# Kernel tuning notes

Measured on AMD Instinct MI355X. Metric: run time of the kernel, lower is better.

Reference implementation:

```python
import jax, jax.numpy as jnp
import numpy as np

N_NODES = 50000
N_EDGES = 600000
D = 128
DROP_P = 0.5


def setup_inputs() -> dict:
    key = jax.random.key(0)
    k1, k2, k3, k4, k5, k6 = jax.random.split(key, 6)
    x = jax.random.normal(k1, (N_NODES, D), dtype=jnp.float32)
    W = jax.random.normal(k2, (D, D), dtype=jnp.float32) * (1.0 / np.sqrt(D))
    b = jax.random.normal(k3, (D,), dtype=jnp.float32) * 0.01
    mask_u = jax.random.uniform(k4, (N_NODES, D), dtype=jnp.float32)
    src = jax.random.randint(k5, (N_EDGES,), 0, N_NODES, dtype=jnp.int64)
    dst = jax.random.randint(k6, (N_EDGES,), 0, N_NODES, dtype=jnp.int64)
    return {"x": x, "W": W, "b": b, "mask_u": mask_u, "src": src, "dst": dst}


def reference(x, W, b, mask_u, src, dst):
    n_nodes = x.shape[0]
    # linear + relu (nn.Linear stores weight as [out, in]; here W is [out, in])
    h = jax.nn.relu(jnp.einsum('nd,od->no', x, W) + b)
    # inverted dropout with precomputed uniform noise (train mode, p=0.5)
    keep = (mask_u >= DROP_P).astype(h.dtype)
    h = h * keep * (1.0 / (1.0 - DROP_P))
    # message passing: msg = h[src], reduce = sum over incoming edges per dst
    msgs = jnp.take(h, src, axis=0)            # [E, D] gather
    out = jax.ops.segment_sum(msgs, dst, num_segments=n_nodes)  # [N, D]
    return out
```

## Files before the change

### kernel.cpp

```cpp
#include <hip/hip_runtime.h>

#define D 128
#define TILE_N 16
#define HPITCH 132
#define CAP 32
#define SPILL_MAX 8192

typedef __attribute__((ext_vector_type(8))) short  short8;
typedef __attribute__((ext_vector_type(4))) float  f32x4;

__device__ inline unsigned short f32_to_bf16(float f) {
    unsigned int u = __float_as_uint(f);
    unsigned int r = (u + 0x7FFFu + ((u >> 16) & 1u)) >> 16;
    return (unsigned short)r;
}
__device__ inline float bf16_to_f32(unsigned short s) {
    return __uint_as_float(((unsigned int)s) << 16);
}
__device__ inline short8 pack_bf16x8(float4 a, float4 b) {
    short8 u;
    u[0] = (short)f32_to_bf16(a.x); u[1] = (short)f32_to_bf16(a.y);
    u[2] = (short)f32_to_bf16(a.z); u[3] = (short)f32_to_bf16(a.w);
    u[4] = (short)f32_to_bf16(b.x); u[5] = (short)f32_to_bf16(b.y);
    u[6] = (short)f32_to_bf16(b.z); u[7] = (short)f32_to_bf16(b.w);
    return u;
}

__global__ __launch_bounds__(256) void prep_kernel(
    const float* __restrict__ W, unsigned short* __restrict__ Wb,
    const float* __restrict__ x, unsigned short* __restrict__ xb,
    const float* __restrict__ mask_u, unsigned char* __restrict__ mbits,
    int* __restrict__ cnt, int n_nodes, int* __restrict__ spill_cnt)
{
    const int tid = blockIdx.x * 256 + threadIdx.x;
    const int nth = gridDim.x * 256;

    for (int i = tid; i < (D * D) / 8; i += nth) {
        float4 v0 = *(const float4*)&W[i * 8];
        float4 v1 = *(const float4*)&W[i * 8 + 4];
        *(short8*)&Wb[i * 8] = pack_bf16x8(v0, v1);
    }
    const int nx8 = n_nodes * (D / 8);
    for (int i = tid; i < nx8; i += nth) {
        float4 v0 = *(const float4*)&x[(size_t)i * 8];
        float4 v1 = *(const float4*)&x[(size_t)i * 8 + 4];
        *(short8*)&xb[(size_t)i * 8] = pack_bf16x8(v0, v1);
    }
    for (int i = tid; i < nx8; i += nth) {
        float4 m0 = *(const float4*)&mask_u[(size_t)i * 8];
        float4 m1 = *(const float4*)&mask_u[(size_t)i * 8 + 4];
        unsigned b = 0;
        b |= (m0.x >= 0.5f) ? 1u : 0u;   b |= (m0.y >= 0.5f) ? 2u : 0u;
        b |= (m0.z >= 0.5f) ? 4u : 0u;   b |= (m0.w >= 0.5f) ? 8u : 0u;
        b |= (m1.x >= 0.5f) ? 16u : 0u;  b |= (m1.y >= 0.5f) ? 32u : 0u;
        b |= (m1.z >= 0.5f) ? 64u : 0u;  b |= (m1.w >= 0.5f) ? 128u : 0u;
        mbits[i] = (unsigned char)b;
    }
    for (int i = tid; i < n_nodes; i += nth) cnt[i] = 0;
    if (tid == 0 && spill_cnt) *spill_cnt = 0;
}

__global__ __launch_bounds__(256, 8) void gemm_mfma_kernel(
    const unsigned short* __restrict__ xb, const unsigned short* __restrict__ Wb,
    const float* __restrict__ bias, const unsigned char* __restrict__ mbits,
    unsigned short* __restrict__ h, int n_nodes,
    const int* __restrict__ src, const int* __restrict__ dst, int n_edges,
    int* __restrict__ cnt, unsigned short* __restrict__ bucket,
    int* __restrict__ spill_cnt, int* __restrict__ spill)
{
    __shared__ unsigned short ht[TILE_N * HPITCH];
    const int t    = threadIdx.x;
    const int lane = t & 63;
    const int w    = t >> 6;
    const int fr   = lane & 15;
    const int fg   = lane >> 4;
    const int n0 = blockIdx.x * TILE_N;

    const int e0 = blockIdx.x * 256 + t;
    int e_dst = 0, e_src = 0;
    const bool has_e0 = (e0 < n_edges);
    if (has_e0) { e_dst = dst[e0]; e_src = src[e0]; }

    const int prow = t >> 4;
    const int pcg  = t & 15;
    const int pnode = n0 + prow;
    const bool pvalid = (pnode < n_nodes);
    unsigned mbyte = 0;
    if (pvalid) mbyte = mbits[pnode * 16 + pcg];

    int arow = n0 + fr;
    if (arow >= n_nodes) arow = n_nodes - 1;
    const unsigned short* xr = xb + (size_t)arow * D;
    short8 a0 = *(const short8*)&xr[ 0 + fg * 8];
    short8 a1 = *(const short8*)&xr[32 + fg * 8];
    short8 a2 = *(const short8*)&xr[64 + fg * 8];
    short8 a3 = *(const short8*)&xr[96 + fg * 8];

    const float bs0 = bias[32 * w + fr];
    const float bs1 = bias[32 * w + 16 + fr];

    const unsigned short* wb0 = Wb + (size_t)(32 * w + fr) * D;
    const unsigned short* wb1 = Wb + (size_t)(32 * w + 16 + fr) * D;

    f32x4 acc0 = (f32x4){0.f, 0.f, 0.f, 0.f};
    f32x4 acc1 = (f32x4){0.f, 0.f, 0.f, 0.f};
    #pragma unroll
    for (int s = 0; s < 4; ++s) {
        short8 a = (s == 0) ? a0 : (s == 1) ? a1 : (s == 2) ? a2 : a3;
        short8 b0 = *(const short8*)&wb0[s * 32 + fg * 8];
        short8 b1 = *(const short8*)&wb1[s * 32 + fg * 8];
        acc0 = __builtin_amdgcn_mfma_f32_16x16x32_bf16(a, b0, acc0, 0, 0, 0);
        acc1 = __builtin_amdgcn_mfma_f32_16x16x32_bf16(a, b1, acc1, 0, 0, 0);
    }

    #pragma unroll
    for (int r = 0; r < 4; ++r) {
        const int rl = fg * 4 + r;
        float v0 = fmaxf(acc0[r] + bs0, 0.f);
        float v1 = fmaxf(acc1[r] + bs1, 0.f);
        ht[rl * HPITCH + 32 * w + fr]      = f32_to_bf16(v0);
        ht[rl * HPITCH + 32 * w + 16 + fr] = f32_to_bf16(v1);
    }
    __syncthreads();

    if (has_e0) {
        int pos = atomicAdd(&cnt[e_dst], 1);
        if (pos < CAP) {
            bucket[(size_t)e_dst * CAP + pos] = (unsigned short)e_src;
        } else {
            int k = atomicAdd(spill_cnt, 1);
            if (k < SPILL_MAX) { spill[2 * k] = e_dst; spill[2 * k + 1] = e_src; }
        }
    }
    const int stride = gridDim.x * 256;
    for (int i = e0 + stride; i < n_edges; i += stride) {
        int dd  = dst[i];
        int ss  = src[i];
        int pos = atomicAdd(&cnt[dd], 1);
        if (pos < CAP) {
            bucket[(size_t)dd * CAP + pos] = (unsigned short)ss;
        } else {
            int k = atomicAdd(spill_cnt, 1);
            if (k < SPILL_MAX) { spill[2 * k] = dd; spill[2 * k + 1] = ss; }
        }
    }

    if (pvalid) {
        short8 hv = *(const short8*)&ht[prow * HPITCH + pcg * 8];
        short8 o;
        #pragma unroll
        for (int j = 0; j < 8; ++j) {
            float v = bf16_to_f32((unsigned short)hv[j]) * 2.f;
            o[j] = ((mbyte >> j) & 1u) ? (short)f32_to_bf16(v) : (short)0;
        }
        *(short8*)&h[(size_t)pnode * D + pcg * 8] = o;
    }
}

__global__ __launch_bounds__(256) void gather_reduce_kernel(
    const unsigned short* __restrict__ h, const int* __restrict__ cnt,
    const unsigned short* __restrict__ bucket, float* __restrict__ out,
    int n_nodes)
{
    const int t = threadIdx.x;
    const int node = blockIdx.x * 16 + (t >> 4);
    if (node >= n_nodes) return;
    const int cb = (t & 15) * 8;
    int deg = cnt[node];
    if (deg > CAP) deg = CAP;
    const unsigned short* b = bucket + (size_t)node * CAP;

    float acc[8];
    #pragma unroll
    for (int j = 0; j < 8; ++j) acc[j] = 0.f;

    int i = 0;
    for (; i + 3 < deg; i += 4) {
        int s0 = b[i], s1 = b[i + 1], s2 = b[i + 2], s3 = b[i + 3];
        short8 v0 = *(const short8*)&h[(size_t)s0 * D + cb];
        short8 v1 = *(const short8*)&h[(size_t)s1 * D + cb];
        short8 v2 = *(const short8*)&h[(size_t)s2 * D + cb];
        short8 v3 = *(const short8*)&h[(size_t)s3 * D + cb];
        #pragma unroll
        for (int j = 0; j < 8; ++j)
            acc[j] += (bf16_to_f32((unsigned short)v0[j]) +
                       bf16_to_f32((unsigned short)v1[j])) +
                      (bf16_to_f32((unsigned short)v2[j]) +
                       bf16_to_f32((unsigned short)v3[j]));
    }
    for (; i < deg; ++i) {
        int s0 = b[i];
        short8 v0 = *(const short8*)&h[(size_t)s0 * D + cb];
        #pragma unroll
        for (int j = 0; j < 8; ++j) acc[j] += bf16_to_f32((unsigned short)v0[j]);
    }

    f32x4 o0 = (f32x4){acc[0], acc[1], acc[2], acc[3]};
    f32x4 o1 = (f32x4){acc[4], acc[5], acc[6], acc[7]};
    __builtin_nontemporal_store(o0, (f32x4*)&out[(size_t)node * D + cb]);
    __builtin_nontemporal_store(o1, (f32x4*)&out[(size_t)node * D + cb + 4]);
}

__global__ __launch_bounds__(256) void spill_apply_kernel(
    const unsigned short* __restrict__ h, const int* __restrict__ spill_cnt,
    const int* __restrict__ spill, float* __restrict__ out)
{
    int n = *spill_cnt;
    if (n > SPILL_MAX) n = SPILL_MAX;
    for (int e = threadIdx.x / 16; e < n; e += 16) {
        int dd = spill[2 * e], ss = spill[2 * e + 1];
        int cb = (threadIdx.x & 15) * 8;
        short8 v = *(const short8*)&h[(size_t)ss * D + cb];
        float* o = &out[(size_t)dd * D + cb];
        #pragma unroll
        for (int j = 0; j < 8; ++j)
            atomicAdd(o + j, bf16_to_f32((unsigned short)v[j]));
    }
}

__global__ __launch_bounds__(256) void zero_kernel(int* __restrict__ p, int n)
{
    int i = blockIdx.x * 256 + threadIdx.x;
    if (i < n) p[i] = 0;
}

__global__ __launch_bounds__(256) void gemm_fb_kernel(
    const float* __restrict__ x, const float* __restrict__ W,
    const float* __restrict__ bias, const float* __restrict__ mask_u,
    unsigned short* __restrict__ h, int n_nodes)
{
    int tid = blockIdx.x * 256 + threadIdx.x;
    if (tid >= n_nodes * 16) return;
    int node = tid >> 4, cg = tid & 15;
    for (int c = 0; c < 8; ++c) {
        int col = cg * 8 + c;
        float s = bias[col];
        for (int k = 0; k < D; ++k)
            s += bf16_to_f32(f32_to_bf16(x[(size_t)node * D + k])) *
                 bf16_to_f32(f32_to_bf16(W[(size_t)col * D + k]));
        s = fmaxf(s, 0.f);
        float m = mask_u[(size_t)node * D + col];
        s *= (m >= 0.5f) ? 2.f : 0.f;
        h[(size_t)node * D + col] = f32_to_bf16(s);
    }
}

__global__ __launch_bounds__(256) void scatter_atomic_kernel(
    const unsigned short* __restrict__ h, const int* __restrict__ src,
    const int* __restrict__ dst, float* __restrict__ out, int n_edges)
{
    const int t = threadIdx.x;
    const int e = blockIdx.x * 16 + (t >> 4);
    if (e >= n_edges) return;
    const int cb = (t & 15) * 8;
    const int s  = src[e];
    const int dd = dst[e];
    short8 v = *(const short8*)&h[(size_t)s * D + cb];
    float* o = &out[(size_t)dd * D + cb];
    #pragma unroll
    for (int j = 0; j < 8; ++j) atomicAdd(o + j, bf16_to_f32((unsigned short)v[j]));
}

extern "C" void kernel_launch(void* const* d_in, const int* in_sizes, int n_in,
                              void* d_out, int out_size, void* d_ws, size_t ws_size,
                              hipStream_t stream) {
    const float* x      = (const float*)d_in[0];
    const float* W      = (const float*)d_in[1];
    const float* bias   = (const float*)d_in[2];
    const float* mask_u = (const float*)d_in[3];
    const int*   src    = (const int*)d_in[4];
    const int*   dst    = (const int*)d_in[5];
    float* out = (float*)d_out;

    const int n_nodes = in_sizes[0] / D;
    const int n_edges = in_sizes[4];
    const int n_tiles = (n_nodes + TILE_N - 1) / TILE_N;

    const size_t wb_bytes = (size_t)D * D * sizeof(unsigned short);
    const size_t xb_bytes = (size_t)n_nodes * D * sizeof(unsigned short);
    const size_t h_bytes  = (size_t)n_nodes * D * sizeof(unsigned short);
    unsigned short* Wb = (unsigned short*)d_ws;
    unsigned short* xb = (unsigned short*)((char*)d_ws + wb_bytes);
    unsigned short* h  = (unsigned short*)((char*)d_ws + wb_bytes + xb_bytes);
    int* cnt       = (int*)((char*)d_ws + wb_bytes + xb_bytes + h_bytes);
    int* spill_cnt = cnt + n_nodes;
    int* spill     = spill_cnt + 1;
    unsigned short* bucket = (unsigned short*)(spill + 2 * SPILL_MAX);
    unsigned char*  mbits  = (unsigned char*)(bucket + (size_t)n_nodes * CAP);
    const size_t needed = wb_bytes + xb_bytes + h_bytes +
        ((size_t)n_nodes + 1 + 2 * SPILL_MAX) * sizeof(int) +
        (size_t)n_nodes * CAP * sizeof(unsigned short) +
        (size_t)n_nodes * 16;

    if (ws_size >= needed && n_nodes <= 65535) {
        prep_kernel<<<2048, 256, 0, stream>>>(
            W, Wb, x, xb, mask_u, mbits, cnt, n_nodes, spill_cnt);
        gemm_mfma_kernel<<<n_tiles, 256, 0, stream>>>(
            xb, Wb, bias, mbits, h, n_nodes,
            src, dst, n_edges, cnt, bucket, spill_cnt, spill);
        gather_reduce_kernel<<<(n_nodes + 15) / 16, 256, 0, stream>>>(
            h, cnt, bucket, out, n_nodes);
        spill_apply_kernel<<<1, 256, 0, stream>>>(h, spill_cnt, spill, out);
    } else {
        unsigned short* hf = (unsigned short*)d_ws;
        gemm_fb_kernel<<<(n_nodes * 16 + 255) / 256, 256, 0, stream>>>(
            x, W, bias, mask_u, hf, n_nodes);
        zero_kernel<<<(out_size + 255) / 256, 256, 0, stream>>>((int*)d_out, out_size);
        scatter_atomic_kernel<<<(n_edges + 15) / 16, 256, 0, stream>>>(
            hf, src, dst, out, n_edges);
    }
}
```

Before: 78.94 us.

## Bin edges per node range in LDS inside a fused GEMM/binning kernel

Converts src/dst to 16-bit arrays in the prep kernel. Adds binning blocks that each scan the entire edge list and bucket the edges whose destinations fall in their 256-node range, using LDS atomics. They then write the bucket rows and degrees coalesced, which replaces the global atomic counters and scattered bucket writes. These blocks run in the same launch as the GEMM tiles. The cost is that every binning block re-reads the whole dst array, so total edge reads grow with the number of node ranges.

Result: slower. 250.7 us (+217.6%).

```diff
diff --git a/kernel.cpp b/kernel.cpp
--- a/kernel.cpp
+++ b/kernel.cpp
@@ -3,7 +3,7 @@
 #define D 128
 #define TILE_N 16
 #define HPITCH 132
-#define CAP 32
+#define LCAP 32
 #define SPILL_MAX 8192
 
 typedef __attribute__((ext_vector_type(8))) short  short8;
@@ -30,7 +30,9 @@
     const float* __restrict__ W, unsigned short* __restrict__ Wb,
     const float* __restrict__ x, unsigned short* __restrict__ xb,
     const float* __restrict__ mask_u, unsigned char* __restrict__ mbits,
-    int* __restrict__ cnt, int n_nodes, int* __restrict__ spill_cnt)
+    const int* __restrict__ dst, unsigned short* __restrict__ dst16,
+    const int* __restrict__ src, unsigned short* __restrict__ src16,
+    int n_edges, int n_nodes, int* __restrict__ spill_cnt)
 {
     const int tid = blockIdx.x * 256 + threadIdx.x;
     const int nth = gridDim.x * 256;
@@ -56,109 +58,140 @@
         b |= (m1.z >= 0.5f) ? 64u : 0u;  b |= (m1.w >= 0.5f) ? 128u : 0u;
         mbits[i] = (unsigned char)b;
     }
-    for (int i = tid; i < n_nodes; i += nth) cnt[i] = 0;
-    if (tid == 0 && spill_cnt) *spill_cnt = 0;
-}
-
-__global__ __launch_bounds__(256, 8) void gemm_mfma_kernel(
+    for (int i = tid; i < n_edges; i += nth) {
+        dst16[i] = (unsigned short)dst[i];
+        src16[i] = (unsigned short)src[i];
+    }
+    if (tid == 0) *spill_cnt = 0;
+}
+
+__global__ __launch_bounds__(256, 8) void mega_kernel(
     const unsigned short* __restrict__ xb, const unsigned short* __restrict__ Wb,
     const float* __restrict__ bias, const unsigned char* __restrict__ mbits,
     unsigned short* __restrict__ h, int n_nodes,
-    const int* __restrict__ src, const int* __restrict__ dst, int n_edges,
-    int* __restrict__ cnt, unsigned short* __restrict__ bucket,
-    int* __restrict__ spill_cnt, int* __restrict__ spill)
-{
-    __shared__ unsigned short ht[TILE_N * HPITCH];
-    const int t    = threadIdx.x;
-    const int lane = t & 63;
-    const int w    = t >> 6;
-    const int fr   = lane & 15;
-    const int fg   = lane >> 4;
-    const int n0 = blockIdx.x * TILE_N;
-
-    const int e0 = blockIdx.x * 256 + t;
-    int e_dst = 0, e_src = 0;
-    const bool has_e0 = (e0 < n_edges);
-    if (has_e0) { e_dst = dst[e0]; e_src = src[e0]; }
-
-    const int prow = t >> 4;
-    const int pcg  = t & 15;
-    const int pnode = n0 + prow;
-    const bool pvalid = (pnode < n_nodes);
-    unsigned mbyte = 0;
-    if (pvalid) mbyte = mbits[pnode * 16 + pcg];
-
-    int arow = n0 + fr;
-    if (arow >= n_nodes) arow = n_nodes - 1;
-    const unsigned short* xr = xb + (size_t)arow * D;
-    short8 a0 = *(const short8*)&xr[ 0 + fg * 8];
-    short8 a1 = *(const short8*)&xr[32 + fg * 8];
-    short8 a2 = *(const short8*)&xr[64 + fg * 8];
-    short8 a3 = *(const short8*)&xr[96 + fg * 8];
-
-    const float bs0 = bias[32 * w + fr];
-    const float bs1 = bias[32 * w + 16 + fr];
-
-    const unsigned short* wb0 = Wb + (size_t)(32 * w + fr) * D;
-    const unsigned short* wb1 = Wb + (size_t)(32 * w + 16 + fr) * D;
-
-    f32x4 acc0 = (f32x4){0.f, 0.f, 0.f, 0.f};
-    f32x4 acc1 = (f32x4){0.f, 0.f, 0.f, 0.f};
-    #pragma unroll
-    for (int s = 0; s < 4; ++s) {
-        short8 a = (s == 0) ? a0 : (s == 1) ? a1 : (s == 2) ? a2 : a3;
-        short8 b0 = *(const short8*)&wb0[s * 32 + fg * 8];
-        short8 b1 = *(const short8*)&wb1[s * 32 + fg * 8];
-        acc0 = __builtin_amdgcn_mfma_f32_16x16x32_bf16(a, b0, acc0, 0, 0, 0);
-        acc1 = __builtin_amdgcn_mfma_f32_16x16x32_bf16(a, b1, acc1, 0, 0, 0);
-    }
-
-    #pragma unroll
-    for (int r = 0; r < 4; ++r) {
-        const int rl = fg * 4 + r;
-        float v0 = fmaxf(acc0[r] + bs0, 0.f);
-        float v1 = fmaxf(acc1[r] + bs1, 0.f);
-        ht[rl * HPITCH + 32 * w + fr]      = f32_to_bf16(v0);
-        ht[rl * HPITCH + 32 * w + 16 + fr] = f32_to_bf16(v1);
-    }
-    __syncthreads();
-
-    if (has_e0) {
-        int pos = atomicAdd(&cnt[e_dst], 1);
-        if (pos < CAP) {
-            bucket[(size_t)e_dst * CAP + pos] = (unsigned short)e_src;
-        } else {
-            int k = atomicAdd(spill_cnt, 1);
-            if (k < SPILL_MAX) { spill[2 * k] = e_dst; spill[2 * k + 1] = e_src; }
-        }
-    }
-    const int stride = gridDim.x * 256;
-    for (int i = e0 + stride; i < n_edges; i += stride) {
-        int dd  = dst[i];
-        int ss  = src[i];
-        int pos = atomicAdd(&cnt[dd], 1);
-        if (pos < CAP) {
-            bucket[(size_t)dd * CAP + pos] = (unsigned short)ss;
-        } else {
-            int k = atomicAdd(spill_cnt, 1);
-            if (k < SPILL_MAX) { spill[2 * k] = dd; spill[2 * k + 1] = ss; }
-        }
-    }
-
-    if (pvalid) {
-        short8 hv = *(const short8*)&ht[prow * HPITCH + pcg * 8];
-        short8 o;
-        #pragma unroll
-        for (int j = 0; j < 8; ++j) {
-            float v = bf16_to_f32((unsigned short)hv[j]) * 2.f;
-            o[j] = ((mbyte >> j) & 1u) ? (short)f32_to_bf16(v) : (short)0;
-        }
-        *(short8*)&h[(size_t)pnode * D + pcg * 8] = o;
+    const unsigned short* __restrict__ dst16,
+    const unsigned short* __restrict__ src16, int n_edges,
+    int* __restrict__ deg, unsigned short* __restrict__ bucket,
+    int* __restrict__ spill_cnt, int* __restrict__ spill, int nb_bin)
+{
+    __shared__ __align__(16) char smem[17408];
+    const int t = threadIdx.x;
+
+    if ((int)blockIdx.x < nb_bin) {
+        int* s_cnt = (int*)smem;
+        unsigned short* s_slots = (unsigned short*)(smem + 1024);
+        const unsigned rbase = blockIdx.x * 256;
+        s_cnt[t] = 0;
+        __syncthreads();
+
+        const int n8 = n_edges >> 3;
+        for (int i8 = t; i8 < n8; i8 += 256) {
+            short8 d8 = *(const short8*)&dst16[i8 * 8];
+            #pragma unroll
+            for (int j = 0; j < 8; ++j) {
+                unsigned dd  = (unsigned short)d8[j];
+                unsigned rel = dd - rbase;
+                if (rel < 256u) {
+                    int ss = src16[i8 * 8 + j];
+                    int pos = atomicAdd(&s_cnt[rel], 1);
+                    if (pos < LCAP) {
+                        s_slots[(rel << 5) + pos] = (unsigned short)ss;
+                    } else {
+                        int k = atomicAdd(spill_cnt, 1);
+                        if (k < SPILL_MAX) { spill[2 * k] = (int)dd; spill[2 * k + 1] = ss; }
+                    }
+                }
+            }
+        }
+        for (int i = (n8 << 3) + t; i < n_edges; i += 256) {
+            unsigned dd  = dst16[i];
+            unsigned rel = dd - rbase;
+            if (rel < 256u) {
+                int ss = src16[i];
+                int pos = atomicAdd(&s_cnt[rel], 1);
+                if (pos < LCAP) {
+                    s_slots[(rel << 5) + pos] = (unsigned short)ss;
+                } else {
+                    int k = atomicAdd(spill_cnt, 1);
+                    if (k < SPILL_MAX) { spill[2 * k] = (int)dd; spill[2 * k + 1] = ss; }
+                }
+            }
+        }
+        __syncthreads();
+
+        const int node = (int)rbase + t;
+        if (node < n_nodes) deg[node] = s_cnt[t];
+        for (int v = t; v < 1024; v += 256) {
+            int rel = v >> 2;
+            int gn  = (int)rbase + rel;
+            if (gn < n_nodes)
+                *(short8*)&bucket[((size_t)gn << 5) + ((v & 3) << 3)] =
+                    *(const short8*)&s_slots[v << 3];
+        }
+    } else {
+        unsigned short* ht = (unsigned short*)smem;
+        const int lane = t & 63;
+        const int w    = t >> 6;
+        const int fr   = lane & 15;
+        const int fg   = lane >> 4;
+        const int n0 = (blockIdx.x - nb_bin) * TILE_N;
+
+        const int prow = t >> 4;
+        const int pcg  = t & 15;
+        const int pnode = n0 + prow;
+        const bool pvalid = (pnode < n_nodes);
+        unsigned mbyte = 0;
+        if (pvalid) mbyte = mbits[pnode * 16 + pcg];
+
+        int arow = n0 + fr;
+        if (arow >= n_nodes) arow = n_nodes - 1;
+        const unsigned short* xr = xb + (size_t)arow * D;
+        short8 a0 = *(const short8*)&xr[ 0 + fg * 8];
+        short8 a1 = *(const short8*)&xr[32 + fg * 8];
+        short8 a2 = *(const short8*)&xr[64 + fg * 8];
+        short8 a3 = *(const short8*)&xr[96 + fg * 8];
+
+        const float bs0 = bias[32 * w + fr];
+        const float bs1 = bias[32 * w + 16 + fr];
+        const unsigned short* wb0 = Wb + (size_t)(32 * w + fr) * D;
+        const unsigned short* wb1 = Wb + (size_t)(32 * w + 16 + fr) * D;
+
+        f32x4 acc0 = (f32x4){0.f, 0.f, 0.f, 0.f};
+        f32x4 acc1 = (f32x4){0.f, 0.f, 0.f, 0.f};
+        #pragma unroll
+        for (int s = 0; s < 4; ++s) {
+            short8 a = (s == 0) ? a0 : (s == 1) ? a1 : (s == 2) ? a2 : a3;
+            short8 b0 = *(const short8*)&wb0[s * 32 + fg * 8];
+            short8 b1 = *(const short8*)&wb1[s * 32 + fg * 8];
+            acc0 = __builtin_amdgcn_mfma_f32_16x16x32_bf16(a, b0, acc0, 0, 0, 0);
+            acc1 = __builtin_amdgcn_mfma_f32_16x16x32_bf16(a, b1, acc1, 0, 0, 0);
+        }
+
+        #pragma unroll
+        for (int r = 0; r < 4; ++r) {
+            const int rl = fg * 4 + r;
+            float v0 = fmaxf(acc0[r] + bs0, 0.f);
+            float v1 = fmaxf(acc1[r] + bs1, 0.f);
+            ht[rl * HPITCH + 32 * w + fr]      = f32_to_bf16(v0);
+            ht[rl * HPITCH + 32 * w + 16 + fr] = f32_to_bf16(v1);
+        }
+        __syncthreads();
+
+        if (pvalid) {
+            short8 hv = *(const short8*)&ht[prow * HPITCH + pcg * 8];
+            short8 o;
+            #pragma unroll
+            for (int j = 0; j < 8; ++j) {
+                float v = bf16_to_f32((unsigned short)hv[j]) * 2.f;
+                o[j] = ((mbyte >> j) & 1u) ? (short)f32_to_bf16(v) : (short)0;
+            }
+            *(short8*)&h[(size_t)pnode * D + pcg * 8] = o;
+        }
     }
 }
 
 __global__ __launch_bounds__(256) void gather_reduce_kernel(
-    const unsigned short* __restrict__ h, const int* __restrict__ cnt,
+    const unsigned short* __restrict__ h, const int* __restrict__ deg,
     const unsigned short* __restrict__ bucket, float* __restrict__ out,
     int n_nodes)
 {
@@ -166,16 +199,16 @@
     const int node = blockIdx.x * 16 + (t >> 4);
     if (node >= n_nodes) return;
     const int cb = (t & 15) * 8;
-    int deg = cnt[node];
-    if (deg > CAP) deg = CAP;
-    const unsigned short* b = bucket + (size_t)node * CAP;
+    int dg = deg[node];
+    if (dg > LCAP) dg = LCAP;
+    const unsigned short* b = bucket + ((size_t)node << 5);
 
     float acc[8];
     #pragma unroll
     for (int j = 0; j < 8; ++j) acc[j] = 0.f;
 
     int i = 0;
-    for (; i + 3 < deg; i += 4) {
+    for (; i + 3 < dg; i += 4) {
         int s0 = b[i], s1 = b[i + 1], s2 = b[i + 2], s3 = b[i + 3];
         short8 v0 = *(const short8*)&h[(size_t)s0 * D + cb];
         short8 v1 = *(const short8*)&h[(size_t)s1 * D + cb];
@@ -188,7 +221,7 @@
                       (bf16_to_f32((unsigned short)v2[j]) +
                        bf16_to_f32((unsigned short)v3[j]));
     }
-    for (; i < deg; ++i) {
+    for (; i < dg; ++i) {
         int s0 = b[i];
         short8 v0 = *(const short8*)&h[(size_t)s0 * D + cb];
         #pragma unroll
@@ -207,7 +240,7 @@
 {
     int n = *spill_cnt;
     if (n > SPILL_MAX) n = SPILL_MAX;
-    for (int e = threadIdx.x / 16; e < n; e += 16) {
+    for (int e = (int)(threadIdx.x >> 4); e < n; e += 16) {
         int dd = spill[2 * e], ss = spill[2 * e + 1];
         int cb = (threadIdx.x & 15) * 8;
         short8 v = *(const short8*)&h[(size_t)ss * D + cb];
@@ -275,31 +308,33 @@
     const int n_nodes = in_sizes[0] / D;
     const int n_edges = in_sizes[4];
     const int n_tiles = (n_nodes + TILE_N - 1) / TILE_N;
+    const int nb_bin  = (n_nodes + 255) / 256;
 
     const size_t wb_bytes = (size_t)D * D * sizeof(unsigned short);
     const size_t xb_bytes = (size_t)n_nodes * D * sizeof(unsigned short);
     const size_t h_bytes  = (size_t)n_nodes * D * sizeof(unsigned short);
-    unsigned short* Wb = (unsigned short*)d_ws;
-    unsigned short* xb = (unsigned short*)((char*)d_ws + wb_bytes);
-    unsigned short* h  = (unsigned short*)((char*)d_ws + wb_bytes + xb_bytes);
-    int* cnt       = (int*)((char*)d_ws + wb_bytes + xb_bytes + h_bytes);
-    int* spill_cnt = cnt + n_nodes;
-    int* spill     = spill_cnt + 1;
-    unsigned short* bucket = (unsigned short*)(spill + 2 * SPILL_MAX);
-    unsigned char*  mbits  = (unsigned char*)(bucket + (size_t)n_nodes * CAP);
-    const size_t needed = wb_bytes + xb_bytes + h_bytes +
-        ((size_t)n_nodes + 1 + 2 * SPILL_MAX) * sizeof(int) +
-        (size_t)n_nodes * CAP * sizeof(unsigned short) +
-        (size_t)n_nodes * 16;
+    char* p = (char*)d_ws;
+    unsigned short* Wb = (unsigned short*)p;            p += wb_bytes;
+    unsigned short* xb = (unsigned short*)p;            p += xb_bytes;
+    unsigned short* h  = (unsigned short*)p;            p += h_bytes;
+    int* deg       = (int*)p;                           p += (size_t)((n_nodes + 3) & ~3) * sizeof(int);
+    int* spill_cnt = (int*)p;                           p += 16;
+    int* spill     = (int*)p;                           p += (size_t)2 * SPILL_MAX * sizeof(int);
+    unsigned short* bucket = (unsigned short*)p;        p += (size_t)n_nodes * LCAP * sizeof(unsigned short);
+    unsigned short* dst16  = (unsigned short*)p;        p += (size_t)((n_edges + 7) & ~7) * sizeof(unsigned short);
+    unsigned short* src16  = (unsigned short*)p;        p += (size_t)((n_edges + 7) & ~7) * sizeof(unsigned short);
+    unsigned char*  mbits  = (unsigned char*)p;         p += (size_t)n_nodes * 16;
+    const size_t needed = (size_t)(p - (char*)d_ws);
 
     if (ws_size >= needed && n_nodes <= 65535) {
         prep_kernel<<<2048, 256, 0, stream>>>(
-            W, Wb, x, xb, mask_u, mbits, cnt, n_nodes, spill_cnt);
-        gemm_mfma_kernel<<<n_tiles, 256, 0, stream>>>(
+            W, Wb, x, xb, mask_u, mbits, dst, dst16, src, src16,
+            n_edges, n_nodes, spill_cnt);
+        mega_kernel<<<nb_bin + n_tiles, 256, 0, stream>>>(
             xb, Wb, bias, mbits, h, n_nodes,
-            src, dst, n_edges, cnt, bucket, spill_cnt, spill);
+            dst16, src16, n_edges, deg, bucket, spill_cnt, spill, nb_bin);
         gather_reduce_kernel<<<(n_nodes + 15) / 16, 256, 0, stream>>>(
-            h, cnt, bucket, out, n_nodes);
+            h, deg, bucket, out, n_nodes);
         spill_apply_kernel<<<1, 256, 0, stream>>>(h, spill_cnt, spill, out);
     } else {
         unsigned short* hf = (unsigned short*)d_ws;
```
